# Optimization experiments

Hardware: AMD Instinct MI355X
Metric: run time of the kernel (lower is better)

The kernel has to match this reference:

```python
import math
import jax, jax.numpy as jnp
import numpy as np


def setup_inputs() -> dict:
    key = jax.random.key(0)
    k1, k2 = jax.random.split(key)
    x = jax.random.normal(k1, (32, 3, 64, 64), dtype=jnp.float32)   # (B,C,H,W)
    y = jax.random.normal(k2, (512, 3, 64, 64), dtype=jnp.float32)  # (N,C,H,W)
    return {"x": x, "y": y}


def reference(x, y):
    # Faithful to torch rfft/irfft with normalized=True (unitary / 'ortho' scaling).
    B, C, H, W = x.shape
    scale = math.sqrt(H * W)  # self.N in the torch module
    X = jnp.fft.rfft2(x, norm="ortho")  # (B,C,H,W//2+1) complex
    Y = jnp.fft.rfft2(y, norm="ortho")  # (N,C,H,W//2+1) complex
    # conj(X) . Y summed over channels, fused as one complex contraction
    G = jnp.einsum("bchw,nchw->bnhw", jnp.conj(X), Y)  # (B,N,H,W//2+1)
    g = jnp.fft.irfft2(G, s=(H, W), norm="ortho") * scale  # (B,N,H,W)
    m = jnp.max(g, axis=(-2, -1))  # MaxPool2d(kernel=input_size) -> (B,N)
    xx = jnp.linalg.norm(x.reshape(B, -1), axis=-1)[:, None]  # (B,1)
    yy = jnp.linalg.norm(y.reshape(y.shape[0], -1), axis=-1)[None, :]  # (1,N)
    return m / xx / yy
```

## Files before the change

kernel.cpp:

```cpp
#include <hip/hip_runtime.h>
#include <math.h>

#define FBINS 2112
#define CSC 66
#define NPB 4

typedef float cplx __attribute__((ext_vector_type(2)));
typedef __fp16 half2v __attribute__((ext_vector_type(2)));
#define MK2(a,b) (cplx){(float)(a), (float)(b)}

__device__ __forceinline__ cplx shufxy(cplx a){ return __builtin_shufflevector(a, a, 1, 0); }
template<int S> __device__ __forceinline__ cplx imul(cplx a){
    return (S > 0) ? shufxy(a) * MK2(-1.f, 1.f) : shufxy(a) * MK2(1.f, -1.f);
}
template<int S> __device__ __forceinline__ cplx cmul_tw(cplx a, cplx w){
    cplx ws = shufxy(w);
    return (S > 0) ? a.x*w + a.y*(ws*MK2(-1.f, 1.f))
                   : a.x*(w*MK2(1.f, -1.f)) + a.y*ws;
}

__device__ __forceinline__ unsigned pack16(float a, float b){
    half2v h = __builtin_amdgcn_cvt_pkrtz(a, b);
    return __builtin_bit_cast(unsigned, h);
}
__device__ __forceinline__ half2v h2(unsigned u){ return __builtin_bit_cast(half2v, u); }
__device__ __forceinline__ float fdot2(half2v a, half2v b, float c){
#if __has_builtin(__builtin_amdgcn_fdot2)
    return __builtin_amdgcn_fdot2(a, b, c, false);
#else
    return c + (float)a.x*(float)b.x + (float)a.y*(float)b.y;
#endif
}
__device__ __forceinline__ void dotw(unsigned ux, unsigned uy, float& r, float& s){
    unsigned xs = ((ux >> 16) | (ux << 16)) ^ 0x00008000u;
    r = fdot2(h2(ux), h2(uy), r);
    s = fdot2(h2(xs), h2(uy), s);
}
__device__ __forceinline__ void dotw_i(unsigned ux, unsigned uy, cplx& v){
    float rr = 0.f, ss = 0.f;
    dotw(ux, uy, rr, ss);
    v += MK2(-ss, rr);
}

__device__ __constant__ float TWC[112] = {
  1.f,0.f, 1.f,0.f, 1.f,0.f, 1.f,0.f, 1.f,0.f, 1.f,0.f, 1.f,0.f,
  0.9951847267f,0.0980171403f, 0.9807852804f,0.1950903220f, 0.9569403357f,0.2902846773f,
  0.9238795325f,0.3826834324f, 0.8819212643f,0.4713967368f, 0.8314696123f,0.5555702330f,
  0.7730104534f,0.6343932842f,
  0.9807852804f,0.1950903220f, 0.9238795325f,0.3826834324f, 0.8314696123f,0.5555702330f,
  0.7071067812f,0.7071067812f, 0.5555702330f,0.8314696123f, 0.3826834324f,0.9238795325f,
  0.1950903220f,0.9807852804f,
  0.9569403357f,0.2902846773f, 0.8314696123f,0.5555702330f, 0.6343932842f,0.7730104534f,
  0.3826834324f,0.9238795325f, 0.0980171403f,0.9951847267f, -0.1950903220f,0.9807852804f,
  -0.4713967368f,0.8819212643f,
  0.9238795325f,0.3826834324f, 0.7071067812f,0.7071067812f, 0.3826834324f,0.9238795325f,
  0.f,1.f, -0.3826834324f,0.9238795325f, -0.7071067812f,0.7071067812f,
  -0.9238795325f,0.3826834324f,
  0.8819212643f,0.4713967368f, 0.5555702330f,0.8314696123f, 0.0980171403f,0.9951847267f,
  -0.3826834324f,0.9238795325f, -0.7730104534f,0.6343932842f, -0.9807852804f,0.1950903220f,
  -0.9569403357f,-0.2902846773f,
  0.8314696123f,0.5555702330f, 0.3826834324f,0.9238795325f, -0.1950903220f,0.9807852804f,
  -0.7071067812f,0.7071067812f, -0.9807852804f,0.1950903220f, -0.9238795325f,-0.3826834324f,
  -0.5555702330f,-0.8314696123f,
  0.7730104534f,0.6343932842f, 0.1950903220f,0.9807852804f, -0.4713967368f,0.8819212643f,
  -0.9238795325f,0.3826834324f, -0.9569403357f,-0.2902846773f, -0.5555702330f,-0.8314696123f,
  0.0980171403f,-0.9951847267f
};
__device__ __forceinline__ void load_tw(int j, cplx wj[7]){
    #pragma unroll
    for (int k=0;k<7;++k) wj[k] = MK2(TWC[(j*7+k)*2], TWC[(j*7+k)*2+1]);
}

template<int S>
__device__ __forceinline__ void dft8(cplx v[8]) {
    const float C = 0.70710678118654752440f;
    cplx t0=v[0]+v[4], t4=v[0]-v[4];
    cplx t1=v[1]+v[5], t5=v[1]-v[5];
    cplx t2=v[2]+v[6], t6=v[2]-v[6];
    cplx t3=v[3]+v[7], t7=v[3]-v[7];
    cplx u0=t0+t2, u2=t0-t2;
    cplx u1=t1+t3, u3=t1-t3;
    v[0]=u0+u1; v[4]=u0-u1;
    cplx m3=imul<S>(u3);
    v[2]=u2+m3; v[6]=u2-m3;
    cplx z0=t4;
    cplx z1 = C*(t5 + imul<S>(t5));
    cplx z2 = imul<S>(t6);
    cplx z3 = C*(imul<S>(t7) - t7);
    cplx w0=z0+z2, w2=z0-z2;
    cplx w1=z1+z3, w3=z1-z3;
    v[1]=w0+w1; v[5]=w0-w1;
    cplx mb=imul<S>(w3);
    v[3]=w2+mb; v[7]=w2-mb;
}

template<int S>
__device__ __forceinline__ void fft64_from_regs(
    cplx v[8], cplx* __restrict__ mem, int base, int j, const cplx wj[7])
{
    dft8<S>(v);
    #pragma unroll
    for (int k=1;k<8;++k) v[k] = cmul_tw<S>(v[k], wj[k-1]);
    #pragma unroll
    for (int k=0;k<8;++k) mem[base + 8*j + (k^j)] = v[k];
    #pragma unroll
    for (int n=0;n<8;++n) v[n] = mem[base + 8*n + (j^n)];
    dft8<S>(v);
}

__global__ __launch_bounds__(256) void fwd_fft_kernel(
    const float* __restrict__ x, const float* __restrict__ y,
    unsigned* __restrict__ Xh, unsigned* __restrict__ Yh,
    float* __restrict__ pn)
{
    __shared__ __align__(16) cplx CL[2176];
    __shared__ float red[4];
    const int tid = threadIdx.x, G = tid>>3, j = tid&7;
    const int blk = blockIdx.x;
    const bool isX = blk < 96;

    cplx wj[7]; load_tw(j, wj);

    const float* img = (isX ? x + (size_t)blk * 4096
                            : y + (size_t)(blk - 96) * 4096);
    unsigned* o = (isX ? Xh + (size_t)blk * FBINS
                       : Yh + (size_t)(blk - 96) * FBINS);

    {
        cplx v[8];
        float ns = 0.f;
        #pragma unroll
        for (int nn=0;nn<8;++nn){ int w=8*nn+j;
            float a = img[64*G + w], c = img[64*(G+32) + w];
            v[nn] = MK2(a, c);
            ns = fmaf(a, a, ns); ns = fmaf(c, c, ns); }
        #pragma unroll
        for (int off = 32; off; off >>= 1) ns += __shfl_xor(ns, off);
        if ((tid & 63) == 0) red[tid >> 6] = ns;
        int base = CSC*G;
        fft64_from_regs<-1>(v, CL, base, j, wj);
        #pragma unroll
        for (int k=0;k<8;++k) CL[base + j + 8*k] = v[k];
    }
    __syncthreads();

    {
        cplx v[8];
        if (G == 0) {
            #pragma unroll
            for (int nn=0;nn<8;++nn){
                int r=8*nn+j, p=r&31, hi=r>>5;
                cplx a0  = CL[CSC*p + 0];
                cplx a32 = CL[CSC*p + 32];
                v[nn] = hi ? MK2(a0.y, a32.y) : MK2(a0.x, a32.x);
            }
        } else {
            const int c = G;
            #pragma unroll
            for (int nn=0;nn<8;++nn){
                int r=8*nn+j, p=r&31, hi=r>>5;
                cplx A  = CL[CSC*p + c];
                cplx Bm = CL[CSC*p + 64 - c];
                if (!hi) v[nn] = 0.5f*(A + Bm*MK2(1.f,-1.f));
                else     v[nn] = 0.5f*(shufxy(A)*MK2(1.f,-1.f) + shufxy(Bm));
            }
        }
        __syncthreads();
        int base = CSC*G;
        fft64_from_regs<-1>(v, CL, base, j, wj);
        #pragma unroll
        for (int k=0;k<8;++k) CL[base + j + 8*k] = v[k];
    }
    __syncthreads();

    for (int i = tid; i < FBINS; i += 256) {
        int wp = i>>6, h = i&63;
        cplx r;
        if (wp == 0) {
            int h2i = (64-h)&63;
            cplx av = CL[h], bb = CL[h2i];
            r = 0.5f*(av + bb*MK2(1.f,-1.f));
        } else if (wp == 32) {
            int h2i = (64-h)&63;
            cplx av = CL[h], bb = CL[h2i];
            r = 0.5f*(shufxy(av)*MK2(1.f,-1.f) + shufxy(bb));
        } else {
            r = CL[CSC*wp + h];
        }
        int slot = (wp << 6) | ((h & 7) << 3) | (h >> 3);
        o[slot] = pack16(r.x, r.y);
    }
    if (tid == 0) pn[blk] = red[0] + red[1] + red[2] + red[3];
}

__global__ __launch_bounds__(256) void corr_kernel(
    const unsigned* __restrict__ Xh, const unsigned* __restrict__ Yh,
    const float* __restrict__ px, const float* __restrict__ py,
    float* __restrict__ out)
{
    __shared__ __align__(16) cplx CL[2176];
    __shared__ float red[4];
    const int tid = threadIdx.x, G = tid>>3, j = tid&7;

    const int blk = blockIdx.x;
    const int xcd = blk & 7, idx = blk >> 3;
    const int n  = xcd*64 + (idx & 63);
    const int bg = idx >> 6;

    cplx wj[7]; load_tw(j, wj);
    const int base = CSC*G;

    const float y2 = py[3*n] + py[3*n+1] + py[3*n+2];

    const uint4* pY4 = (const uint4*)Yh + (size_t)n * 3 * 528;
    uint4 yv[3][2];
    {
        const int off = 16*G + 2*j;
        #pragma unroll
        for (int ch=0; ch<3; ++ch){
            yv[ch][0] = pY4[ch*528 + off];
            yv[ch][1] = pY4[ch*528 + off + 1];
        }
    }

    for (int q = 0; q < NPB; ++q) {
        const int b = bg*NPB + q;
        const uint4* pX4 = (const uint4*)Xh + (size_t)b * 3 * 528;

        cplx v[8];
        {
            float r[8], s[8];
            #pragma unroll
            for (int k=0;k<8;++k){ r[k]=0.f; s[k]=0.f; }
            const int off = 16*G + 2*j;
            #pragma unroll
            for (int ch = 0; ch < 3; ++ch) {
                uint4 x0 = pX4[ch*528 + off], x1 = pX4[ch*528 + off + 1];
                dotw(x0.x, yv[ch][0].x, r[0], s[0]);  dotw(x0.y, yv[ch][0].y, r[1], s[1]);
                dotw(x0.z, yv[ch][0].z, r[2], s[2]);  dotw(x0.w, yv[ch][0].w, r[3], s[3]);
                dotw(x1.x, yv[ch][1].x, r[4], s[4]);  dotw(x1.y, yv[ch][1].y, r[5], s[5]);
                dotw(x1.z, yv[ch][1].z, r[6], s[6]);  dotw(x1.w, yv[ch][1].w, r[7], s[7]);
            }
            #pragma unroll
            for (int k=0;k<8;++k) v[k] = MK2(r[k], s[k]);
        }
        if (G == 0) {
            const int off = 512 + 2*j;
            #pragma unroll
            for (int ch = 0; ch < 3; ++ch) {
                uint4 x0 = pX4[ch*528 + off], x1 = pX4[ch*528 + off + 1];
                uint4 y0 = pY4[ch*528 + off], y1 = pY4[ch*528 + off + 1];
                dotw_i(x0.x, y0.x, v[0]);  dotw_i(x0.y, y0.y, v[1]);
                dotw_i(x0.z, y0.z, v[2]);  dotw_i(x0.w, y0.w, v[3]);
                dotw_i(x1.x, y1.x, v[4]);  dotw_i(x1.y, y1.y, v[5]);
                dotw_i(x1.z, y1.z, v[6]);  dotw_i(x1.w, y1.w, v[7]);
            }
        }

        fft64_from_regs<1>(v, CL, base, j, wj);
        #pragma unroll
        for (int k=0;k<4;++k)
            *(float4*)&CL[base + 2*(j+8*k)] =
                make_float4(v[k].x, v[k].y, v[k+4].x, v[k+4].y);
        __syncthreads();

        float m = -3.4e38f;
        {
            if (j == 0) {
                float4 f = *(float4*)&CL[2*G];
                v[0] = MK2(f.x, f.z);
                v[4] = MK2(f.y, f.w);
            } else {
                float4 f = *(float4*)&CL[CSC*j + 2*G];
                v[0] = MK2(f.x,f.y) + imul<1>(MK2(f.z,f.w));
                float4 g2 = *(float4*)&CL[CSC*(32-j) + 2*G];
                v[4] = MK2(g2.x,g2.y)*MK2(1.f,-1.f) + shufxy(MK2(g2.z,g2.w));
            }
            #pragma unroll
            for (int nn=1;nn<4;++nn){
                int w = 8*nn + j;
                float4 f = *(float4*)&CL[CSC*w + 2*G];
                v[nn] = MK2(f.x,f.y) + imul<1>(MK2(f.z,f.w));
            }
            #pragma unroll
            for (int nn=5;nn<8;++nn){
                int w2 = 64 - (8*nn + j);
                float4 f = *(float4*)&CL[CSC*w2 + 2*G];
                v[nn] = MK2(f.x,f.y)*MK2(1.f,-1.f) + shufxy(MK2(f.z,f.w));
            }
            __syncthreads();
            fft64_from_regs<1>(v, CL, base, j, wj);
            #pragma unroll
            for (int k=0;k<8;++k) m = fmaxf(m, fmaxf(v[k].x, v[k].y));
        }
        #pragma unroll
        for (int off = 32; off; off >>= 1) m = fmaxf(m, __shfl_xor(m, off));
        if ((tid & 63) == 0) red[tid >> 6] = m;
        __syncthreads();
        if (tid == 0) {
            const float x2 = px[3*b] + px[3*b+1] + px[3*b+2];
            const float dinv = rsqrtf(x2 * y2) * (1.0f/4096.0f);
            float mm = fmaxf(fmaxf(red[0], red[1]), fmaxf(red[2], red[3]));
            out[b*512 + n] = mm * dinv;
        }
    }
}

extern "C" void kernel_launch(void* const* d_in, const int* in_sizes, int n_in,
                              void* d_out, int out_size, void* d_ws, size_t ws_size,
                              hipStream_t stream) {
    const float* x = (const float*)d_in[0];
    const float* y = (const float*)d_in[1];
    float* out = (float*)d_out;

    unsigned* Xh = (unsigned*)d_ws;
    unsigned* Yh = Xh + 96 * FBINS;
    float* pn = (float*)(Yh + 1536 * FBINS);
    float* px = pn;
    float* py = pn + 96;

    fwd_fft_kernel<<<1632, 256, 0, stream>>>(x, y, Xh, Yh, pn);
    corr_kernel<<<32/NPB*512, 256, 0, stream>>>(Xh, Yh, px, py, out);
}
```

Baseline: 90.01 us.

## Re-tile correlation kernel to two N per block, vectorize LDS transpose stores

The correlation grid changes from 4 batch images per block reusing one cached Y spectrum (4096 blocks) to one batch image and two Y items per block (8192 blocks). X is now held constant per block, so Y is reloaded per pair instead of per block. The transpose store inside the FFT now writes float4 pairs instead of scalar complex stores, and the swap/negate in the dot helper moves from the X operand to the Y operand. This aims for more parallelism and wider LDS writes, at the cost of more Y global traffic and a different reuse pattern.

```diff
diff --git a/kernel.cpp b/kernel.cpp
--- a/kernel.cpp
+++ b/kernel.cpp
@@ -3,7 +3,6 @@
 
 #define FBINS 2112
 #define CSC 66
-#define NPB 4
 
 typedef float cplx __attribute__((ext_vector_type(2)));
 typedef __fp16 half2v __attribute__((ext_vector_type(2)));
@@ -32,9 +31,9 @@
 #endif
 }
 __device__ __forceinline__ void dotw(unsigned ux, unsigned uy, float& r, float& s){
-    unsigned xs = ((ux >> 16) | (ux << 16)) ^ 0x00008000u;
+    unsigned ys = ((uy >> 16) | (uy << 16)) ^ 0x80000000u;
     r = fdot2(h2(ux), h2(uy), r);
-    s = fdot2(h2(xs), h2(uy), s);
+    s = fdot2(h2(ux), h2(ys), s);
 }
 __device__ __forceinline__ void dotw_i(unsigned ux, unsigned uy, cplx& v){
     float rr = 0.f, ss = 0.f;
@@ -102,7 +101,10 @@
     #pragma unroll
     for (int k=1;k<8;++k) v[k] = cmul_tw<S>(v[k], wj[k-1]);
     #pragma unroll
-    for (int k=0;k<8;++k) mem[base + 8*j + (k^j)] = v[k];
+    for (int t=0;t<8;t+=2){
+        cplx lo = v[t^j], hi = v[(t|1)^j];
+        *(float4*)&mem[base + 8*j + t] = make_float4(lo.x, lo.y, hi.x, hi.y);
+    }
     #pragma unroll
     for (int n=0;n<8;++n) v[n] = mem[base + 8*n + (j^n)];
     dft8<S>(v);
@@ -204,52 +206,44 @@
 
     const int blk = blockIdx.x;
     const int xcd = blk & 7, idx = blk >> 3;
-    const int n  = xcd*64 + (idx & 63);
-    const int bg = idx >> 6;
+    const int n0 = xcd*64 + ((idx & 31) << 1);
+    const int b  = idx >> 5;
 
     cplx wj[7]; load_tw(j, wj);
     const int base = CSC*G;
-
-    const float y2 = py[3*n] + py[3*n+1] + py[3*n+2];
-
-    const uint4* pY4 = (const uint4*)Yh + (size_t)n * 3 * 528;
-    uint4 yv[3][2];
-    {
-        const int off = 16*G + 2*j;
-        #pragma unroll
-        for (int ch=0; ch<3; ++ch){
-            yv[ch][0] = pY4[ch*528 + off];
-            yv[ch][1] = pY4[ch*528 + off + 1];
-        }
-    }
-
-    for (int q = 0; q < NPB; ++q) {
-        const int b = bg*NPB + q;
-        const uint4* pX4 = (const uint4*)Xh + (size_t)b * 3 * 528;
+    const int offA = 16*G + 2*j;
+    const int off32 = 512 + 2*j;
+
+    const uint4* pX4 = (const uint4*)Xh + (size_t)b * 3 * 528;
+    const float x2 = px[3*b] + px[3*b+1] + px[3*b+2];
+
+    #pragma unroll
+    for (int q = 0; q < 2; ++q) {
+        const int n = n0 + q;
+        const uint4* pY4 = (const uint4*)Yh + (size_t)n * 3 * 528;
 
         cplx v[8];
         {
             float r[8], s[8];
             #pragma unroll
             for (int k=0;k<8;++k){ r[k]=0.f; s[k]=0.f; }
-            const int off = 16*G + 2*j;
             #pragma unroll
             for (int ch = 0; ch < 3; ++ch) {
-                uint4 x0 = pX4[ch*528 + off], x1 = pX4[ch*528 + off + 1];
-                dotw(x0.x, yv[ch][0].x, r[0], s[0]);  dotw(x0.y, yv[ch][0].y, r[1], s[1]);
-                dotw(x0.z, yv[ch][0].z, r[2], s[2]);  dotw(x0.w, yv[ch][0].w, r[3], s[3]);
-                dotw(x1.x, yv[ch][1].x, r[4], s[4]);  dotw(x1.y, yv[ch][1].y, r[5], s[5]);
-                dotw(x1.z, yv[ch][1].z, r[6], s[6]);  dotw(x1.w, yv[ch][1].w, r[7], s[7]);
+                uint4 x0 = pX4[ch*528 + offA], x1 = pX4[ch*528 + offA + 1];
+                uint4 y0 = pY4[ch*528 + offA], y1 = pY4[ch*528 + offA + 1];
+                dotw(x0.x, y0.x, r[0], s[0]);  dotw(x0.y, y0.y, r[1], s[1]);
+                dotw(x0.z, y0.z, r[2], s[2]);  dotw(x0.w, y0.w, r[3], s[3]);
+                dotw(x1.x, y1.x, r[4], s[4]);  dotw(x1.y, y1.y, r[5], s[5]);
+                dotw(x1.z, y1.z, r[6], s[6]);  dotw(x1.w, y1.w, r[7], s[7]);
             }
             #pragma unroll
             for (int k=0;k<8;++k) v[k] = MK2(r[k], s[k]);
         }
         if (G == 0) {
-            const int off = 512 + 2*j;
             #pragma unroll
             for (int ch = 0; ch < 3; ++ch) {
-                uint4 x0 = pX4[ch*528 + off], x1 = pX4[ch*528 + off + 1];
-                uint4 y0 = pY4[ch*528 + off], y1 = pY4[ch*528 + off + 1];
+                uint4 x0 = pX4[ch*528 + off32], x1 = pX4[ch*528 + off32 + 1];
+                uint4 y0 = pY4[ch*528 + off32], y1 = pY4[ch*528 + off32 + 1];
                 dotw_i(x0.x, y0.x, v[0]);  dotw_i(x0.y, y0.y, v[1]);
                 dotw_i(x0.z, y0.z, v[2]);  dotw_i(x0.w, y0.w, v[3]);
                 dotw_i(x1.x, y1.x, v[4]);  dotw_i(x1.y, y1.y, v[5]);
@@ -298,7 +292,7 @@
         if ((tid & 63) == 0) red[tid >> 6] = m;
         __syncthreads();
         if (tid == 0) {
-            const float x2 = px[3*b] + px[3*b+1] + px[3*b+2];
+            const float y2 = py[3*n] + py[3*n+1] + py[3*n+2];
             const float dinv = rsqrtf(x2 * y2) * (1.0f/4096.0f);
             float mm = fmaxf(fmaxf(red[0], red[1]), fmaxf(red[2], red[3]));
             out[b*512 + n] = mm * dinv;
@@ -320,5 +314,5 @@
     float* py = pn + 96;
 
     fwd_fft_kernel<<<1632, 256, 0, stream>>>(x, y, Xh, Yh, pn);
-    corr_kernel<<<32/NPB*512, 256, 0, stream>>>(Xh, Yh, px, py, out);
-}
+    corr_kernel<<<8192, 256, 0, stream>>>(Xh, Yh, px, py, out);
+}
```

After: 166.3 us. +84.8%, slower.
